# Optimization experiments

Measured on AMD Instinct MI355X. Metric: run time of the kernel, lower is better.

## Reference

```python
import jax, jax.numpy as jnp
import numpy as np

N_NEURONS = 256
P_MAX = 8
N_BLOCKS = P_MAX + 1
HIDDEN = 32
BATCH = 8192


def setup_inputs() -> dict:
    key = jax.random.key(0)
    ks = jax.random.split(key, 9)
    z = jax.random.normal(ks[0], (BATCH, N_BLOCKS * N_NEURONS), dtype=jnp.float32)
    # Per-block ScalarMLP params, stacked over the n_blocks axis.
    s1 = 1.0 / np.sqrt(N_NEURONS)
    s2 = 1.0 / np.sqrt(HIDDEN)
    gW1 = jax.random.uniform(ks[1], (N_BLOCKS, N_NEURONS, HIDDEN), jnp.float32, -s1, s1)
    gb1 = jax.random.uniform(ks[2], (N_BLOCKS, HIDDEN), jnp.float32, -s1, s1)
    gW2 = jax.random.uniform(ks[3], (N_BLOCKS, HIDDEN, HIDDEN), jnp.float32, -s2, s2)
    gb2 = jax.random.uniform(ks[4], (N_BLOCKS, HIDDEN), jnp.float32, -s2, s2)
    gW3 = jax.random.uniform(ks[5], (N_BLOCKS, HIDDEN), jnp.float32, -s2, s2)
    gb3 = jax.random.uniform(ks[6], (N_BLOCKS,), jnp.float32, -s2, s2)
    # Lag coupling matrices W_r ~ U(-init_scale, init_scale), init_scale=0.1
    W = jax.random.uniform(ks[7], (P_MAX, N_NEURONS, N_NEURONS), jnp.float32, -0.1, 0.1)
    return {"z": z, "gW1": gW1, "gb1": gb1, "gW2": gW2, "gb2": gb2,
            "gW3": gW3, "gb3": gb3, "W": W}


def _energy(z, gW1, gb1, gW2, gb2, gW3, gb3, W):
    B = z.shape[0]
    blocks = z.reshape(B, N_BLOCKS, N_NEURONS)           # (B, K, n)
    # Per-block ScalarMLP energies (all blocks at once).
    h1 = jax.nn.silu(jnp.einsum('bkn,knh->bkh', blocks, gW1) + gb1)   # (B, K, H)
    h2 = jax.nn.silu(jnp.einsum('bkh,khg->bkg', h1, gW2) + gb2)       # (B, K, H)
    e = jnp.einsum('bkh,kh->bk', h2, gW3) + gb3                        # (B, K)
    # Bilinear lag couplings: z_future^T W_r z_{lag-r}, r = 1..p_max.
    z_future = blocks[:, P_MAX, :]                                     # (B, n)
    lags = blocks[:, :P_MAX, :][:, ::-1, :]                            # (B, p, n), index r-1 == block p_max-r
    cross = jnp.einsum('bi,rij,brj->b', z_future, W, lags)             # (B,)
    return e.sum(axis=-1) + cross                                      # (B,)


def reference(z, gW1, gb1, gW2, gb2, gW3, gb3, W):
    # Score s(z) = -grad_z U(z); sum over batch gives per-sample grads
    # since energies are independent across samples.
    grad_z = jax.grad(lambda zz: _energy(zz, gW1, gb1, gW2, gb2, gW3, gb3, W).sum())(z)
    return -grad_z
```

## Files before the change

kernel.cpp:

```cpp
#include <hip/hip_runtime.h>
#include <hip/hip_bf16.h>
#include <math.h>

#define BATCH 8192
#define NB 9
#define NN 256
#define PMAX 8
#define HID 32
#define ZDIM 2304

typedef short bf16x8 __attribute__((ext_vector_type(8)));
typedef float f32x4 __attribute__((ext_vector_type(4)));

static __device__ inline unsigned short f2bf(float f) {
    __hip_bfloat16 h = __float2bfloat16(f);
    return *reinterpret_cast<unsigned short*>(&h);
}

static __device__ inline uint4 pack8(float4 a, float4 b) {
    uint4 u;
    u.x = (unsigned)f2bf(a.x) | ((unsigned)f2bf(a.y) << 16);
    u.y = (unsigned)f2bf(a.z) | ((unsigned)f2bf(a.w) << 16);
    u.z = (unsigned)f2bf(b.x) | ((unsigned)f2bf(b.y) << 16);
    u.w = (unsigned)f2bf(b.z) | ((unsigned)f2bf(b.w) << 16);
    return u;
}

__global__ __launch_bounds__(256) void k_pack(
    const float* __restrict__ W, const float* __restrict__ gW1,
    unsigned short* __restrict__ Wb, unsigned short* __restrict__ WTb,
    unsigned short* __restrict__ gW1b, unsigned short* __restrict__ g1Tb) {
    int r = blockIdx.z;
    int t = threadIdx.x;
    if (r < 8) {
        __shared__ float tt[32][33];
        int i0 = blockIdx.y * 32;
        int j0 = blockIdx.x * 32;
        int tx = t & 31;
        int ty = t >> 5;
        const float* src = W + (size_t)r * 65536;
        #pragma unroll
        for (int s = 0; s < 32; s += 8) {
            float v = src[(size_t)(i0 + ty + s) * 256 + (j0 + tx)];
            tt[ty + s][tx] = v;
            Wb[(size_t)r * 65536 + (size_t)(i0 + ty + s) * 256 + (j0 + tx)] = f2bf(v);
        }
        __syncthreads();
        #pragma unroll
        for (int s = 0; s < 32; s += 8)
            WTb[(size_t)r * 65536 + (size_t)(j0 + ty + s) * 256 + (i0 + tx)] = f2bf(tt[tx][ty + s]);
    } else {
        int tg = (blockIdx.y * 8 + blockIdx.x) * 256 + t;
        for (int e = tg; e < 73728; e += 16384) {
            float v = gW1[e];
            unsigned short b = f2bf(v);
            gW1b[e] = b;
            int k = e >> 13, n = (e >> 5) & 255, h = e & 31;
            g1Tb[(size_t)(k * 32 + h) * 256 + n] = b;
        }
    }
}

__global__ __launch_bounds__(256) void k_mlp(
    const float* __restrict__ z, const unsigned short* __restrict__ g1Tb,
    const float* __restrict__ gb1, const float* __restrict__ gW2,
    const float* __restrict__ gb2, const float* __restrict__ gW3,
    float* __restrict__ d1ws) {
    __shared__ uint4 As4[512];
    __shared__ uint4 Bw[1024];
    __shared__ uint4 W2Ts4[128];
    __shared__ uint4 W2Ns4[128];

    int t = threadIdx.x;
    int lane = t & 63;
    int w = t >> 6;
    int k = blockIdx.y;
    int b0 = blockIdx.x * 128;

    const unsigned short* bsrc = g1Tb + (size_t)k * 8192;
    for (int e = t; e < 1024; e += 256) {
        int h = e >> 5;
        int rest = e & 31;
        int c = rest >> 2, q = rest & 3;
        Bw[c * 128 + (h & 15) + 16 * q + 64 * (h >> 4)] =
            *(const uint4*)(bsrc + (size_t)h * 256 + c * 32 + q * 8);
    }
    const float* gw2 = gW2 + (size_t)k * 1024;
    unsigned short* w2t = (unsigned short*)W2Ts4;
    unsigned short* w2n = (unsigned short*)W2Ns4;
    for (int e = t; e < 1024; e += 256) {
        int n = e >> 5, kk = e & 31;
        int q = kk >> 3, jj = kk & 7;
        int ci = (n & 15) + 16 * q + 64 * (n >> 4);
        w2t[ci * 8 + jj] = f2bf(gw2[kk * 32 + n]);
        w2n[ci * 8 + jj] = f2bf(gw2[n * 32 + kk]);
    }

    int mq_m = t >> 2;
    int q = t & 3;

    f32x4 acc1[2][2];
    #pragma unroll
    for (int i = 0; i < 2; ++i)
        #pragma unroll
        for (int j = 0; j < 2; ++j) acc1[i][j] = (f32x4){0.f, 0.f, 0.f, 0.f};

    for (int c = 0; c < 8; ++c) {
        float4 fa[2][2];
        #pragma unroll
        for (int pp = 0; pp < 2; ++pp) {
            int m = mq_m + 64 * pp;
            const float* as = z + (size_t)(b0 + m) * ZDIM + k * 256 + c * 32 + q * 8;
            fa[pp][0] = *(const float4*)(as);
            fa[pp][1] = *(const float4*)(as + 4);
        }
        __syncthreads();
        #pragma unroll
        for (int pp = 0; pp < 2; ++pp) {
            int m = mq_m + 64 * pp;
            As4[(m & 15) + 16 * q + 64 * (m >> 4)] = pack8(fa[pp][0], fa[pp][1]);
        }
        __syncthreads();
        bf16x8 af[2], bfr[2];
        #pragma unroll
        for (int i = 0; i < 2; ++i) af[i] = __builtin_bit_cast(bf16x8, As4[lane + (w * 2 + i) * 64]);
        #pragma unroll
        for (int j = 0; j < 2; ++j) bfr[j] = __builtin_bit_cast(bf16x8, Bw[c * 128 + lane + j * 64]);
        #pragma unroll
        for (int i = 0; i < 2; ++i)
            #pragma unroll
            for (int j = 0; j < 2; ++j)
                acc1[i][j] = __builtin_amdgcn_mfma_f32_16x16x32_bf16(af[i], bfr[j], acc1[i][j], 0, 0, 0);
    }

    int cq = lane >> 4;
    int ci16 = lane & 15;
    float b1v[2], b2v[2], g3v[2];
    #pragma unroll
    for (int j = 0; j < 2; ++j) {
        b1v[j] = gb1[k * 32 + j * 16 + ci16];
        b2v[j] = gb2[k * 32 + j * 16 + ci16];
        g3v[j] = gW3[k * 32 + j * 16 + ci16];
    }
    unsigned short* Hs = (unsigned short*)As4;
    float sp1[2][2][4];
    __syncthreads();
    #pragma unroll
    for (int i = 0; i < 2; ++i)
        #pragma unroll
        for (int j = 0; j < 2; ++j)
            #pragma unroll
            for (int r = 0; r < 4; ++r) {
                float a1 = acc1[i][j][r] + b1v[j];
                float s1 = 1.f / (1.f + __expf(-a1));
                sp1[i][j][r] = s1 * (1.f + a1 * (1.f - s1));
                int row = w * 32 + i * 16 + cq * 4 + r;
                int col = j * 16 + ci16;
                int chunk = (row & 15) + 16 * (col >> 3) + 64 * (row >> 4);
                Hs[chunk * 8 + (col & 7)] = f2bf(a1 * s1);
            }
    __syncthreads();

    bf16x8 af2[2], wf[2];
    #pragma unroll
    for (int i = 0; i < 2; ++i) af2[i] = __builtin_bit_cast(bf16x8, As4[lane + (w * 2 + i) * 64]);
    #pragma unroll
    for (int j = 0; j < 2; ++j) wf[j] = __builtin_bit_cast(bf16x8, W2Ts4[lane + j * 64]);
    f32x4 acc2[2][2];
    #pragma unroll
    for (int i = 0; i < 2; ++i)
        #pragma unroll
        for (int j = 0; j < 2; ++j) {
            acc2[i][j] = (f32x4){0.f, 0.f, 0.f, 0.f};
            acc2[i][j] = __builtin_amdgcn_mfma_f32_16x16x32_bf16(af2[i], wf[j], acc2[i][j], 0, 0, 0);
        }

    __syncthreads();
    #pragma unroll
    for (int i = 0; i < 2; ++i)
        #pragma unroll
        for (int j = 0; j < 2; ++j)
            #pragma unroll
            for (int r = 0; r < 4; ++r) {
                float a2 = acc2[i][j][r] + b2v[j];
                float s2 = 1.f / (1.f + __expf(-a2));
                float da2 = g3v[j] * s2 * (1.f + a2 * (1.f - s2));
                int row = w * 32 + i * 16 + cq * 4 + r;
                int col = j * 16 + ci16;
                int chunk = (row & 15) + 16 * (col >> 3) + 64 * (row >> 4);
                Hs[chunk * 8 + (col & 7)] = f2bf(da2);
            }
    __syncthreads();

    bf16x8 af3[2], wg[2];
    #pragma unroll
    for (int i = 0; i < 2; ++i) af3[i] = __builtin_bit_cast(bf16x8, As4[lane + (w * 2 + i) * 64]);
    #pragma unroll
    for (int j = 0; j < 2; ++j) wg[j] = __builtin_bit_cast(bf16x8, W2Ns4[lane + j * 64]);
    #pragma unroll
    for (int i = 0; i < 2; ++i)
        #pragma unroll
        for (int j = 0; j < 2; ++j) {
            f32x4 a3 = (f32x4){0.f, 0.f, 0.f, 0.f};
            a3 = __builtin_amdgcn_mfma_f32_16x16x32_bf16(af3[i], wg[j], a3, 0, 0, 0);
            #pragma unroll
            for (int r = 0; r < 4; ++r) {
                int row = w * 32 + i * 16 + cq * 4 + r;
                int col = j * 16 + ci16;
                d1ws[((size_t)k * BATCH + b0 + row) * 32 + col] = a3[r] * sp1[i][j][r];
            }
        }
}

__global__ __launch_bounds__(256) void k_gemm_lo(
    const float* __restrict__ z, const float* __restrict__ d1,
    const unsigned short* __restrict__ WTb, const unsigned short* __restrict__ gW1b,
    float* __restrict__ out) {
    __shared__ uint4 As4[512];
    __shared__ uint4 Bs4[512];

    int t = threadIdx.x;
    int lane = t & 63;
    int w = t >> 6;
    int wr = w >> 1, wc = w & 1;
    int b0 = blockIdx.y * 128;
    int n0 = blockIdx.x * 128;
    int k  = n0 >> 8;
    int jb = n0 & 255;

    const float* Amain = z + (size_t)b0 * ZDIM + 2048;
    const float* Aext  = d1 + ((size_t)k * BATCH + b0) * 32;
    const unsigned short* Bmain = WTb + (size_t)(7 - k) * 65536 + (size_t)jb * 256;
    const unsigned short* Bext  = gW1b + ((size_t)k * 256 + jb) * 32;

    int mq_m = t >> 2;
    int q    = t & 3;

    f32x4 acc[4][4];
    #pragma unroll
    for (int i = 0; i < 4; ++i)
        #pragma unroll
        for (int j = 0; j < 4; ++j) acc[i][j] = (f32x4){0.f, 0.f, 0.f, 0.f};

    for (int c = 0; c < 9; ++c) {
        int kb = c * 32;
        float4 fa[2][2];
        uint4 bu[2];
        #pragma unroll
        for (int pp = 0; pp < 2; ++pp) {
            int m = mq_m + 64 * pp;
            const float* as = (c < 8) ? (Amain + (size_t)m * ZDIM + kb + q * 8)
                                      : (Aext + (size_t)m * 32 + q * 8);
            fa[pp][0] = *(const float4*)(as);
            fa[pp][1] = *(const float4*)(as + 4);
            const unsigned short* bs = (c < 8) ? (Bmain + (size_t)m * 256 + kb + q * 8)
                                               : (Bext + (size_t)m * 32 + q * 8);
            bu[pp] = *(const uint4*)(bs);
        }
        __syncthreads();
        #pragma unroll
        for (int pp = 0; pp < 2; ++pp) {
            int m = mq_m + 64 * pp;
            int ci = (m & 15) + 16 * q + 64 * (m >> 4);
            As4[ci] = pack8(fa[pp][0], fa[pp][1]);
            Bs4[ci] = bu[pp];
        }
        __syncthreads();
        bf16x8 af[4], bf[4];
        #pragma unroll
        for (int i = 0; i < 4; ++i) af[i] = __builtin_bit_cast(bf16x8, As4[lane + (wr * 4 + i) * 64]);
        #pragma unroll
        for (int j = 0; j < 4; ++j) bf[j] = __builtin_bit_cast(bf16x8, Bs4[lane + (wc * 4 + j) * 64]);
        #pragma unroll
        for (int i = 0; i < 4; ++i)
            #pragma unroll
            for (int j = 0; j < 4; ++j)
                acc[i][j] = __builtin_amdgcn_mfma_f32_16x16x32_bf16(af[i], bf[j], acc[i][j], 0, 0, 0);
    }

    int rquad = lane >> 4;
    int cidx  = lane & 15;
    #pragma unroll
    for (int i = 0; i < 4; ++i) {
        #pragma unroll
        for (int j = 0; j < 4; ++j) {
            float* o = out + (size_t)(b0 + wr * 64 + i * 16 + rquad * 4) * ZDIM
                     + (k * 256 + jb + wc * 64 + j * 16 + cidx);
            #pragma unroll
            for (int r = 0; r < 4; ++r)
                o[(size_t)r * ZDIM] = -acc[i][j][r];
        }
    }
}

__global__ __launch_bounds__(256) void k_gemm_hi(
    const float* __restrict__ z, const float* __restrict__ d1,
    const unsigned short* __restrict__ Wb, const unsigned short* __restrict__ gW1b,
    float* __restrict__ out) {
    __shared__ uint4 As4[512];
    __shared__ uint4 Bs4[256];

    int t = threadIdx.x;
    int lane = t & 63;
    int w = t >> 6;
    int b0 = blockIdx.y * 128;
    int i0 = blockIdx.x * 64;

    const float* Amain = z + (size_t)b0 * ZDIM;
    const float* Aext  = d1 + ((size_t)8 * BATCH + b0) * 32;
    const unsigned short* Bext = gW1b + (size_t)(8 * 256 + i0) * 32;

    int mq_m = t >> 2;
    int q    = t & 3;

    f32x4 acc[2][4];
    #pragma unroll
    for (int i = 0; i < 2; ++i)
        #pragma unroll
        for (int j = 0; j < 4; ++j) acc[i][j] = (f32x4){0.f, 0.f, 0.f, 0.f};

    for (int c = 0; c < 65; ++c) {
        int kb = c * 32;
        float4 fa[2][2];
        #pragma unroll
        for (int pp = 0; pp < 2; ++pp) {
            int m = mq_m + 64 * pp;
            const float* as = (c < 64) ? (Amain + (size_t)m * ZDIM + kb + q * 8)
                                       : (Aext + (size_t)m * 32 + q * 8);
            fa[pp][0] = *(const float4*)(as);
            fa[pp][1] = *(const float4*)(as + 4);
        }
        int bn = t >> 2;
        uint4 bu;
        if (c < 64) {
            int lag = c >> 3;
            int j0  = kb & 255;
            bu = *(const uint4*)(Wb + (size_t)(7 - lag) * 65536 + (size_t)(i0 + bn) * 256 + j0 + q * 8);
        } else {
            bu = *(const uint4*)(Bext + (size_t)bn * 32 + q * 8);
        }
        __syncthreads();
        #pragma unroll
        for (int pp = 0; pp < 2; ++pp) {
            int m = mq_m + 64 * pp;
            As4[(m & 15) + 16 * q + 64 * (m >> 4)] = pack8(fa[pp][0], fa[pp][1]);
        }
        Bs4[(bn & 15) + 16 * q + 64 * (bn >> 4)] = bu;
        __syncthreads();
        bf16x8 af[2], bf[4];
        #pragma unroll
        for (int i = 0; i < 2; ++i) af[i] = __builtin_bit_cast(bf16x8, As4[lane + (w * 2 + i) * 64]);
        #pragma unroll
        for (int j = 0; j < 4; ++j) bf[j] = __builtin_bit_cast(bf16x8, Bs4[lane + j * 64]);
        #pragma unroll
        for (int i = 0; i < 2; ++i)
            #pragma unroll
            for (int j = 0; j < 4; ++j)
                acc[i][j] = __builtin_amdgcn_mfma_f32_16x16x32_bf16(af[i], bf[j], acc[i][j], 0, 0, 0);
    }

    int rquad = lane >> 4;
    int cidx  = lane & 15;
    #pragma unroll
    for (int i = 0; i < 2; ++i) {
        #pragma unroll
        for (int j = 0; j < 4; ++j) {
            float* o = out + (size_t)(b0 + w * 32 + i * 16 + rquad * 4) * ZDIM
                     + (2048 + i0 + j * 16 + cidx);
            #pragma unroll
            for (int r = 0; r < 4; ++r)
                o[(size_t)r * ZDIM] = -acc[i][j][r];
        }
    }
}

extern "C" void kernel_launch(void* const* d_in, const int* in_sizes, int n_in,
                              void* d_out, int out_size, void* d_ws, size_t ws_size,
                              hipStream_t stream) {
    const float* z   = (const float*)d_in[0];
    const float* gW1 = (const float*)d_in[1];
    const float* gb1 = (const float*)d_in[2];
    const float* gW2 = (const float*)d_in[3];
    const float* gb2 = (const float*)d_in[4];
    const float* gW3 = (const float*)d_in[5];
    const float* W   = (const float*)d_in[7];
    float* out = (float*)d_out;

    float* ws = (float*)d_ws;
    float*          d1ws = ws;
    unsigned short* Wb   = (unsigned short*)(ws + 2359296);
    unsigned short* WTb  = Wb + 524288;
    unsigned short* gW1b = WTb + 524288;
    unsigned short* g1Tb = gW1b + 73728;

    k_pack<<<dim3(8, 8, 9), 256, 0, stream>>>(W, gW1, Wb, WTb, gW1b, g1Tb);
    k_mlp<<<dim3(64, 9), 256, 0, stream>>>(z, g1Tb, gb1, gW2, gb2, gW3, d1ws);
    k_gemm_lo<<<dim3(16, 64), 256, 0, stream>>>(z, d1ws, WTb, gW1b, out);
    k_gemm_hi<<<dim3(4, 64), 256, 0, stream>>>(z, d1ws, Wb, gW1b, out);
}
```

Measured before the change: 241.6 us.

## Split future-block gradient GEMM over lags with atomic accumulation

The long-K gemm for the future block (65 K-chunks over only 256 workgroups) is replaced by a split-K kernel with one workgroup per lag and 128x128 tiles, accumulating partial results into the output with float atomics. The future block's MLP term (d1 x gW1) now comes from gemm_lo, whose grid grows to cover block 8 and which skips the W chunks for that block. This raises parallelism and lets each tile reuse data better, at the cost of eight atomic adds per output element and a dependency on gemm_lo having written the base values first. Correctness relies on the two kernels running in order on the same stream.

After: 264.4 us. 1.09x slower.

```diff
diff --git a/kernel.cpp b/kernel.cpp
--- a/kernel.cpp
+++ b/kernel.cpp
@@ -230,7 +230,7 @@
 
     const float* Amain = z + (size_t)b0 * ZDIM + 2048;
     const float* Aext  = d1 + ((size_t)k * BATCH + b0) * 32;
-    const unsigned short* Bmain = WTb + (size_t)(7 - k) * 65536 + (size_t)jb * 256;
+    const unsigned short* Bmain = WTb + (size_t)((7 - k) & 7) * 65536 + (size_t)jb * 256;
     const unsigned short* Bext  = gW1b + ((size_t)k * 256 + jb) * 32;
 
     int mq_m = t >> 2;
@@ -242,7 +242,8 @@
         #pragma unroll
         for (int j = 0; j < 4; ++j) acc[i][j] = (f32x4){0.f, 0.f, 0.f, 0.f};
 
-    for (int c = 0; c < 9; ++c) {
+    int cstart = (k == 8) ? 8 : 0;
+    for (int c = cstart; c < 9; ++c) {
         int kb = c * 32;
         float4 fa[2][2];
         uint4 bu[2];
@@ -293,67 +294,60 @@
     }
 }
 
-__global__ __launch_bounds__(256) void k_gemm_hi(
-    const float* __restrict__ z, const float* __restrict__ d1,
-    const unsigned short* __restrict__ Wb, const unsigned short* __restrict__ gW1b,
+__global__ __launch_bounds__(256) void k_hi(
+    const float* __restrict__ z, const unsigned short* __restrict__ Wb,
     float* __restrict__ out) {
     __shared__ uint4 As4[512];
-    __shared__ uint4 Bs4[256];
+    __shared__ uint4 Bs4[512];
 
     int t = threadIdx.x;
     int lane = t & 63;
     int w = t >> 6;
-    int b0 = blockIdx.y * 128;
-    int i0 = blockIdx.x * 64;
-
-    const float* Amain = z + (size_t)b0 * ZDIM;
-    const float* Aext  = d1 + ((size_t)8 * BATCH + b0) * 32;
-    const unsigned short* Bext = gW1b + (size_t)(8 * 256 + i0) * 32;
+    int wr = w >> 1, wc = w & 1;
+    int b0 = blockIdx.x * 128;
+    int jb = blockIdx.y * 128;
+    int lg = blockIdx.z;
+
+    const float* Amain = z + (size_t)b0 * ZDIM + lg * 256;
+    const unsigned short* Bmain = Wb + (size_t)(7 - lg) * 65536 + (size_t)jb * 256;
 
     int mq_m = t >> 2;
     int q    = t & 3;
 
-    f32x4 acc[2][4];
-    #pragma unroll
-    for (int i = 0; i < 2; ++i)
+    f32x4 acc[4][4];
+    #pragma unroll
+    for (int i = 0; i < 4; ++i)
         #pragma unroll
         for (int j = 0; j < 4; ++j) acc[i][j] = (f32x4){0.f, 0.f, 0.f, 0.f};
 
-    for (int c = 0; c < 65; ++c) {
+    for (int c = 0; c < 8; ++c) {
         int kb = c * 32;
         float4 fa[2][2];
-        #pragma unroll
-        for (int pp = 0; pp < 2; ++pp) {
-            int m = mq_m + 64 * pp;
-            const float* as = (c < 64) ? (Amain + (size_t)m * ZDIM + kb + q * 8)
-                                       : (Aext + (size_t)m * 32 + q * 8);
+        uint4 bu[2];
+        #pragma unroll
+        for (int pp = 0; pp < 2; ++pp) {
+            int m = mq_m + 64 * pp;
+            const float* as = Amain + (size_t)m * ZDIM + kb + q * 8;
             fa[pp][0] = *(const float4*)(as);
             fa[pp][1] = *(const float4*)(as + 4);
-        }
-        int bn = t >> 2;
-        uint4 bu;
-        if (c < 64) {
-            int lag = c >> 3;
-            int j0  = kb & 255;
-            bu = *(const uint4*)(Wb + (size_t)(7 - lag) * 65536 + (size_t)(i0 + bn) * 256 + j0 + q * 8);
-        } else {
-            bu = *(const uint4*)(Bext + (size_t)bn * 32 + q * 8);
-        }
-        __syncthreads();
-        #pragma unroll
-        for (int pp = 0; pp < 2; ++pp) {
-            int m = mq_m + 64 * pp;
-            As4[(m & 15) + 16 * q + 64 * (m >> 4)] = pack8(fa[pp][0], fa[pp][1]);
-        }
-        Bs4[(bn & 15) + 16 * q + 64 * (bn >> 4)] = bu;
-        __syncthreads();
-        bf16x8 af[2], bf[4];
-        #pragma unroll
-        for (int i = 0; i < 2; ++i) af[i] = __builtin_bit_cast(bf16x8, As4[lane + (w * 2 + i) * 64]);
-        #pragma unroll
-        for (int j = 0; j < 4; ++j) bf[j] = __builtin_bit_cast(bf16x8, Bs4[lane + j * 64]);
-        #pragma unroll
-        for (int i = 0; i < 2; ++i)
+            bu[pp] = *(const uint4*)(Bmain + (size_t)m * 256 + kb + q * 8);
+        }
+        __syncthreads();
+        #pragma unroll
+        for (int pp = 0; pp < 2; ++pp) {
+            int m = mq_m + 64 * pp;
+            int ci = (m & 15) + 16 * q + 64 * (m >> 4);
+            As4[ci] = pack8(fa[pp][0], fa[pp][1]);
+            Bs4[ci] = bu[pp];
+        }
+        __syncthreads();
+        bf16x8 af[4], bf[4];
+        #pragma unroll
+        for (int i = 0; i < 4; ++i) af[i] = __builtin_bit_cast(bf16x8, As4[lane + (wr * 4 + i) * 64]);
+        #pragma unroll
+        for (int j = 0; j < 4; ++j) bf[j] = __builtin_bit_cast(bf16x8, Bs4[lane + (wc * 4 + j) * 64]);
+        #pragma unroll
+        for (int i = 0; i < 4; ++i)
             #pragma unroll
             for (int j = 0; j < 4; ++j)
                 acc[i][j] = __builtin_amdgcn_mfma_f32_16x16x32_bf16(af[i], bf[j], acc[i][j], 0, 0, 0);
@@ -362,14 +356,14 @@
     int rquad = lane >> 4;
     int cidx  = lane & 15;
     #pragma unroll
-    for (int i = 0; i < 2; ++i) {
+    for (int i = 0; i < 4; ++i) {
         #pragma unroll
         for (int j = 0; j < 4; ++j) {
-            float* o = out + (size_t)(b0 + w * 32 + i * 16 + rquad * 4) * ZDIM
-                     + (2048 + i0 + j * 16 + cidx);
+            float* o = out + (size_t)(b0 + wr * 64 + i * 16 + rquad * 4) * ZDIM
+                     + (2048 + jb + wc * 64 + j * 16 + cidx);
             #pragma unroll
             for (int r = 0; r < 4; ++r)
-                o[(size_t)r * ZDIM] = -acc[i][j][r];
+                unsafeAtomicAdd(o + (size_t)r * ZDIM, -acc[i][j][r]);
         }
     }
 }
@@ -395,6 +389,6 @@
 
     k_pack<<<dim3(8, 8, 9), 256, 0, stream>>>(W, gW1, Wb, WTb, gW1b, g1Tb);
     k_mlp<<<dim3(64, 9), 256, 0, stream>>>(z, g1Tb, gb1, gW2, gb2, gW3, d1ws);
-    k_gemm_lo<<<dim3(16, 64), 256, 0, stream>>>(z, d1ws, WTb, gW1b, out);
-    k_gemm_hi<<<dim3(4, 64), 256, 0, stream>>>(z, d1ws, Wb, gW1b, out);
-}
+    k_gemm_lo<<<dim3(18, 64), 256, 0, stream>>>(z, d1ws, WTb, gW1b, out);
+    k_hi<<<dim3(64, 2, 8), 256, 0, stream>>>(z, Wb, out);
+}
```
